# Performance work log

Measured on AMD Instinct MI355X. Metric: run time of the kernel, lower is better.

## Reference

```python
import jax, jax.numpy as jnp
from jax import lax
import numpy as np

B, T, E, D, EMB, O, L, A = 32, 500, 1024, 1024, 256, 5000, 99, 512
IGNORE = -1


def setup_inputs() -> dict:
    key = jax.random.key(0)
    ks = jax.random.split(key, 32)
    hs_pad = jax.random.normal(ks[0], (B, T, E), jnp.float32)
    hlens = jax.random.randint(ks[1], (B,), 250, T + 1).astype(jnp.int32)
    hlens = hlens.at[0].set(T)
    ylens = jax.random.randint(ks[2], (B,), 50, L + 1)
    labels = jax.random.randint(ks[3], (B, L), 0, O - 1)
    ys_pad = jnp.where(jnp.arange(L)[None, :] < ylens[:, None], labels, IGNORE)

    def w(k, shape, fan):
        return jax.random.normal(k, shape, jnp.float32) / np.float32(np.sqrt(fan))

    params = dict(
        embed=w(ks[4], (O, EMB), EMB),
        W1_W=w(ks[5], (EMB, 2 * D), EMB), b1_W=jnp.zeros(2 * D, jnp.float32),
        W1_Wx=w(ks[6], (EMB, D), EMB), b1_Wx=jnp.zeros(D, jnp.float32),
        U1=w(ks[7], (D, 2 * D), D), Ux1=w(ks[8], (D, D), D),
        U2=w(ks[9], (D, 2 * D), D), b2=jnp.zeros(2 * D, jnp.float32),
        Wc=w(ks[10], (E, 2 * D), E),
        Ux2=w(ks[11], (D, D), D), bUx2=jnp.zeros(D, jnp.float32),
        Wcx=w(ks[12], (E, D), E),
        Winit=w(ks[13], (E, D), E), binit=jnp.zeros(D, jnp.float32),
        Ws=w(ks[14], (D, D), D), bs=jnp.zeros(D, jnp.float32),
        Wy=w(ks[15], (EMB, D), EMB),
        We=w(ks[16], (E, D), E),
        Wlogit=w(ks[17], (D // 2, O), D // 2), blogit=jnp.zeros(O, jnp.float32),
        Wenc=w(ks[18], (E, A), E), Wdec=w(ks[19], (D, A), D),
    )
    return {"hs_pad": hs_pad, "hlens": hlens, "ys_pad": ys_pad, **params}


def reference(hs_pad, hlens, ys_pad, embed, W1_W, b1_W, W1_Wx, b1_Wx, U1, Ux1,
              U2, b2, Wc, Ux2, bUx2, Wcx, Winit, binit, Ws, bs, Wy, We,
              Wlogit, blogit, Wenc, Wdec):
    b, t, e = hs_pad.shape
    d = U1.shape[0]
    o = Wlogit.shape[1]
    sos = eos = o - 1
    l = ys_pad.shape[1]
    olen = l + 1

    ylens = jnp.sum(ys_pad != IGNORE, axis=1)                       # [B]
    ys_in = jnp.concatenate(
        [jnp.full((b, 1), sos, ys_pad.dtype),
         jnp.where(ys_pad == IGNORE, eos, ys_pad)], axis=1)          # [B, olen]
    ymask = (jnp.arange(olen)[None, :] < (ylens + 1)[:, None]).astype(hs_pad.dtype)
    cmask = (jnp.arange(t)[None, :] < hlens[:, None]).astype(hs_pad.dtype)

    # mean_init_state: sums all frames (incl. padding, as in original), / hlens
    h0 = (hs_pad.sum(1) / hlens[:, None].astype(hs_pad.dtype)) @ Winit + binit
    alpha0 = cmask / (cmask.sum(1, keepdims=True) + 1e-8)

    eys = embed[ys_in]                                               # [B, olen, EMB]
    sb_ = eys @ W1_W + b1_W                                          # rnn1_W(eys)
    sbx = eys @ W1_Wx + b1_Wx                                        # rnn1_Wx(eys)

    enc_att = jnp.tanh(hs_pad @ Wenc)                                # [B,T,A] precomputed

    def step(carry, xs):
        h_, alpha = carry
        x_, xx_, m_, sb = xs
        # first GRU cell
        pre1 = jax.nn.sigmoid(h_ @ U1 + x_)
        r1, u1 = pre1[:, :d], pre1[:, d:]
        h1 = jnp.tanh((h_ @ Ux1) * r1 + xx_)
        h1 = u1 * h_ + (1.0 - u1) * h1
        h1 = m_[:, None] * h1 + (1.0 - m_)[:, None] * h_
        # masked dot attention
        dq = jnp.tanh(h1 @ Wdec)                                     # [B,A]
        en = jnp.einsum('bta,ba->bt', enc_att, dq)
        en = jnp.where(cmask > 0, en, -1e9)
        w_att = jax.nn.softmax(en, axis=1)
        c = jnp.einsum('bt,bte->be', w_att, hs_pad)                  # [B,E]
        # second (conditioned) GRU cell
        pre2 = jax.nn.sigmoid(h1 @ U2 + b2 + c @ Wc)
        r2, u2 = pre2[:, :d], pre2[:, d:]
        h2 = jnp.tanh((h1 @ Ux2 + bUx2) * r2 + c @ Wcx)
        h2 = u2 * h1 + (1.0 - u2) * h2
        h2 = m_[:, None] * h2 + (1.0 - m_)[:, None] * h1
        # maxout classifier
        logit = h2 @ Ws + bs + sb @ Wy + c @ We                      # [B,D]
        logit = logit.reshape(b, d // 2, 2).max(-1)
        probs = jax.nn.softmax(logit @ Wlogit + blogit, axis=-1)
        return (h2, w_att), probs

    xs = (jnp.swapaxes(sb_, 0, 1), jnp.swapaxes(sbx, 0, 1),
          ymask.T, jnp.swapaxes(eys, 0, 1))
    _, out = lax.scan(step, (h0, alpha0), xs)                        # [olen,B,O]
    return jnp.swapaxes(out, 0, 1)                                   # [B,olen,O]
```

## Files before the change

kernel.cpp:

```cpp
#include <hip/hip_runtime.h>
#include <math.h>

static constexpr int Bb   = 32;
static constexpr int Tt   = 500;
static constexpr int Ee   = 1024;
static constexpr int EMBc = 256;
static constexpr int Oo   = 5000;
static constexpr int Llen = 99;
static constexpr int OLEN = 100;
static constexpr int Aa   = 512;


__global__ void k_ylens(const int* __restrict__ ys, int* __restrict__ ylens) {
    int b = threadIdx.x;
    if (b < Bb) {
        int c = 0;
        for (int i = 0; i < Llen; i++) c += (ys[b * Llen + i] != -1) ? 1 : 0;
        ylens[b] = c;
    }
}

__global__ void k_embed(const int* __restrict__ ys, const float* __restrict__ embed,
                        float* __restrict__ eys) {
    int blk = blockIdx.x;
    int b = blk / OLEN, i = blk % OLEN;
    int id = Oo - 1;
    if (i > 0) {
        int v = ys[b * Llen + i - 1];
        id = (v == -1) ? (Oo - 1) : v;
    }
    eys[(size_t)(b * OLEN + i) * EMBc + threadIdx.x] = embed[(size_t)id * EMBc + threadIdx.x];
}

__global__ void k_hmean(const float* __restrict__ hs, const int* __restrict__ hlens,
                        float* __restrict__ hm) {
    int b = blockIdx.y;
    int e = blockIdx.x * 256 + threadIdx.x;
    float sum = 0.f;
    for (int t = 0; t < Tt; t++) sum += hs[((size_t)b * Tt + t) * Ee + e];
    hm[(size_t)b * Ee + e] = sum / (float)hlens[b];
}

template <int ACT>
__global__ void k_gemm_tiled(const float* __restrict__ Amat, const float* __restrict__ W,
                             const float* __restrict__ bias, float* __restrict__ C,
                             int M, int K, int N) {
    __shared__ float As[16][132];
    __shared__ float Wt[16][68];
    const int tid = threadIdx.x;
    const int row0 = blockIdx.y * 128;
    const int col0 = blockIdx.x * 64;
    const int ty = tid >> 4, tx = tid & 15;
    float acc[8][4] = {};
    for (int kk = 0; kk < K; kk += 16) {
#pragma unroll
        for (int rr = 0; rr < 128; rr += 64) {
            int r = rr + (tid >> 2);
            int c4 = (tid & 3) * 4;
            float4 v = make_float4(0.f, 0.f, 0.f, 0.f);
            if (row0 + r < M) v = *(const float4*)(&Amat[(size_t)(row0 + r) * K + kk + c4]);
            As[c4 + 0][r] = v.x; As[c4 + 1][r] = v.y; As[c4 + 2][r] = v.z; As[c4 + 3][r] = v.w;
        }
        for (int i = tid; i < 16 * 64; i += 256)
            Wt[i >> 6][i & 63] = W[(size_t)(kk + (i >> 6)) * N + col0 + (i & 63)];
        __syncthreads();
#pragma unroll
        for (int k = 0; k < 16; k++) {
            float a[8], bbv[4];
#pragma unroll
            for (int i = 0; i < 8; i++) a[i] = As[k][ty * 8 + i];
#pragma unroll
            for (int j = 0; j < 4; j++) bbv[j] = Wt[k][tx * 4 + j];
#pragma unroll
            for (int i = 0; i < 8; i++)
#pragma unroll
                for (int j = 0; j < 4; j++) acc[i][j] += a[i] * bbv[j];
        }
        __syncthreads();
    }
#pragma unroll
    for (int i = 0; i < 8; i++) {
        int r = row0 + ty * 8 + i;
        if (r < M) {
#pragma unroll
            for (int j = 0; j < 4; j++) {
                int cc = col0 + tx * 4 + j;
                float v = acc[i][j];
                if (bias) v += bias[cc];
                if (ACT == 1) v = tanhf(v);
                C[(size_t)r * N + cc] = v;
            }
        }
    }
}


template <int KC>
__global__ void k_gemm3(const float* __restrict__ x, int ldx,
                        const float* __restrict__ Wga, const float* __restrict__ Wgb,
                        const float* __restrict__ Wxa, const float* __restrict__ Wxb,
                        int kSeg, float* __restrict__ P) {
    __shared__ float xs[Bb][KC];
    const int tid = threadIdx.x;
    const int kc = blockIdx.y;
    const int k0 = kc * KC;
    for (int i = tid; i < Bb * KC; i += 256) {
        int bb = i / KC, k = i - bb * KC;
        xs[bb][k] = x[(size_t)bb * ldx + k0 + k];
    }
    __syncthreads();
    const int tx = tid & 63, ty = tid >> 6;
    const int j = blockIdx.x * 64 + tx;
    const int b0 = ty * 8;
    const bool seg0 = (k0 < kSeg);
    const float* Wg = seg0 ? Wga : Wgb;
    const float* Wx = seg0 ? Wxa : Wxb;
    const int kbase = seg0 ? k0 : (k0 - kSeg);
    float ag[8] = {}, au[8] = {}, ax[8] = {};
    for (int kk = 0; kk < KC; kk++) {
        const float* wgr = Wg + (size_t)(kbase + kk) * 2048;
        const float* wxr = Wx + (size_t)(kbase + kk) * 1024;
        float wg0 = wgr[j], wg1 = wgr[j + 1024], wx0 = wxr[j];
#pragma unroll
        for (int i = 0; i < 8; i++) {
            float xv = xs[b0 + i][kk];
            ag[i] += xv * wg0;
            au[i] += xv * wg1;
            ax[i] += xv * wx0;
        }
    }
#pragma unroll
    for (int i = 0; i < 8; i++) {
        P[(((size_t)kc * 3 + 0) * Bb + b0 + i) * 1024 + j] = ag[i];
        P[(((size_t)kc * 3 + 1) * Bb + b0 + i) * 1024 + j] = au[i];
        P[(((size_t)kc * 3 + 2) * Bb + b0 + i) * 1024 + j] = ax[i];
    }
}

template <int KC>
__global__ void k_gemm1(const float* __restrict__ x, int ldx,
                        const float* __restrict__ Wa, const float* __restrict__ Wb,
                        int kSeg, int N, float* __restrict__ P) {
    __shared__ float xs[Bb][KC];
    const int tid = threadIdx.x;
    const int kc = blockIdx.y;
    const int k0 = kc * KC;
    for (int i = tid; i < Bb * KC; i += 256) {
        int bb = i / KC, k = i - bb * KC;
        xs[bb][k] = x[(size_t)bb * ldx + k0 + k];
    }
    __syncthreads();
    const int tx = tid & 63, ty = tid >> 6;
    const int j = blockIdx.x * 64 + tx;
    const int b0 = ty * 8;
    const bool seg0 = (k0 < kSeg);
    const float* W = seg0 ? Wa : Wb;
    const int kbase = seg0 ? k0 : (k0 - kSeg);
    float acc[8] = {};
    for (int kk = 0; kk < KC; kk++) {
        float w = W[(size_t)(kbase + kk) * N + j];
#pragma unroll
        for (int i = 0; i < 8; i++) acc[i] += xs[b0 + i][kk] * w;
    }
#pragma unroll
    for (int i = 0; i < 8; i++) P[((size_t)kc * Bb + b0 + i) * N + j] = acc[i];
}

__global__ void k_comb1(const float* __restrict__ P, const float* __restrict__ sb,
                        const float* __restrict__ sbx, const float* __restrict__ h,
                        const int* __restrict__ ylens, float* __restrict__ x23, int s) {
    int gid = blockIdx.x * 256 + threadIdx.x;
    int b = gid >> 10, j = gid & 1023;
    float s0 = 0, s1 = 0, sx = 0;
#pragma unroll
    for (int kc = 0; kc < 16; kc++) {
        s0 += P[(((size_t)kc * 3 + 0) * Bb + b) * 1024 + j];
        s1 += P[(((size_t)kc * 3 + 1) * Bb + b) * 1024 + j];
        sx += P[(((size_t)kc * 3 + 2) * Bb + b) * 1024 + j];
    }
    float r = 1.f / (1.f + expf(-(s0 + sb[((size_t)b * OLEN + s) * 2048 + j])));
    float u = 1.f / (1.f + expf(-(s1 + sb[((size_t)b * OLEN + s) * 2048 + 1024 + j])));
    float ht = tanhf(sx * r + sbx[((size_t)b * OLEN + s) * 1024 + j]);
    float hp = h[(size_t)b * 1024 + j];
    float h1 = u * hp + (1.f - u) * ht;
    float m = (s < ylens[b] + 1) ? 1.f : 0.f;
    h1 = m * h1 + (1.f - m) * hp;
    x23[(size_t)b * 2048 + j] = h1;
}

__global__ void k_en(const float* __restrict__ pd, const float* __restrict__ enc,
                     float* __restrict__ en, float* __restrict__ x23) {
    __shared__ float dqs[Aa];
    const int tid = threadIdx.x;
    const int b = blockIdx.y, tt = blockIdx.x;
    if (tid < 128) x23[(size_t)b * 2048 + 1024 + tt * 128 + tid] = 0.f;
    for (int jj = tid; jj < Aa; jj += 256) {
        float sum = 0;
#pragma unroll
        for (int kc = 0; kc < 16; kc++) sum += pd[((size_t)kc * Bb + b) * Aa + jj];
        dqs[jj] = tanhf(sum);
    }
    __syncthreads();
    const int tx = tid & 63, ty = tid >> 6;
    for (int t2 = 0; t2 < 64; t2 += 4) {
        int t = tt * 64 + t2 + ty;
        if (t < Tt) {
            float acc = 0;
            const float* er = enc + ((size_t)b * Tt + t) * Aa;
#pragma unroll
            for (int i = 0; i < 8; i++) acc += er[tx + 64 * i] * dqs[tx + 64 * i];
#pragma unroll
            for (int off = 32; off > 0; off >>= 1) acc += __shfl_down(acc, off, 64);
            if (tx == 0) en[(size_t)b * 512 + t] = acc;
        }
    }
}

__global__ void k_softc(const float* __restrict__ en, const float* __restrict__ hs,
                        const int* __restrict__ hlens, float* __restrict__ x23) {
    __shared__ float wts[Tt];
    __shared__ float red[128];
    const int tid = threadIdx.x;
    const int b = blockIdx.z;
    const int hlen = hlens[b];
    float mx = -1e30f;
    for (int t = tid; t < hlen; t += 128) mx = fmaxf(mx, en[(size_t)b * 512 + t]);
    red[tid] = mx;
    __syncthreads();
    for (int w = 64; w > 0; w >>= 1) {
        if (tid < w) red[tid] = fmaxf(red[tid], red[tid + w]);
        __syncthreads();
    }
    mx = red[0];
    __syncthreads();
    float ps = 0;
    for (int t = tid; t < Tt; t += 128) {
        float w = 0.f;
        if (t < hlen) w = expf(en[(size_t)b * 512 + t] - mx);
        wts[t] = w;
        ps += w;
    }
    red[tid] = ps;
    __syncthreads();
    for (int w = 64; w > 0; w >>= 1) {
        if (tid < w) red[tid] += red[tid + w];
        __syncthreads();
    }
    float inv = 1.f / red[0];
    __syncthreads();
    for (int t = tid; t < Tt; t += 128) wts[t] *= inv;
    __syncthreads();

    const int e0 = blockIdx.x * 512 + tid * 4;
    const int tc = blockIdx.y;
    int tstart = tc * 125;
    int tend = tstart + 125;
    if (tend > hlen) tend = hlen;
    float4 a0 = make_float4(0, 0, 0, 0), a1 = make_float4(0, 0, 0, 0);
    float4 a2 = make_float4(0, 0, 0, 0), a3 = make_float4(0, 0, 0, 0);
    int t = tstart;
    for (; t + 3 < tend; t += 4) {
        float w0 = wts[t], w1 = wts[t + 1], w2 = wts[t + 2], w3 = wts[t + 3];
        float4 h0 = *(const float4*)(&hs[((size_t)b * Tt + t) * Ee + e0]);
        float4 h1 = *(const float4*)(&hs[((size_t)b * Tt + t + 1) * Ee + e0]);
        float4 h2 = *(const float4*)(&hs[((size_t)b * Tt + t + 2) * Ee + e0]);
        float4 h3 = *(const float4*)(&hs[((size_t)b * Tt + t + 3) * Ee + e0]);
        a0.x += w0 * h0.x; a0.y += w0 * h0.y; a0.z += w0 * h0.z; a0.w += w0 * h0.w;
        a1.x += w1 * h1.x; a1.y += w1 * h1.y; a1.z += w1 * h1.z; a1.w += w1 * h1.w;
        a2.x += w2 * h2.x; a2.y += w2 * h2.y; a2.z += w2 * h2.z; a2.w += w2 * h2.w;
        a3.x += w3 * h3.x; a3.y += w3 * h3.y; a3.z += w3 * h3.z; a3.w += w3 * h3.w;
    }
    for (; t < tend; t++) {
        float w = wts[t];
        float4 hv = *(const float4*)(&hs[((size_t)b * Tt + t) * Ee + e0]);
        a0.x += w * hv.x; a0.y += w * hv.y; a0.z += w * hv.z; a0.w += w * hv.w;
    }
    a0.x += a1.x + a2.x + a3.x;
    a0.y += a1.y + a2.y + a3.y;
    a0.z += a1.z + a2.z + a3.z;
    a0.w += a1.w + a2.w + a3.w;
    float* cdst = &x23[(size_t)b * 2048 + 1024 + e0];
    atomicAdd(cdst + 0, a0.x);
    atomicAdd(cdst + 1, a0.y);
    atomicAdd(cdst + 2, a0.z);
    atomicAdd(cdst + 3, a0.w);
}

__global__ void k_comb2(const float* __restrict__ P, const float* __restrict__ b2,
                        const float* __restrict__ bUx2, const int* __restrict__ ylens,
                        float* __restrict__ x23, float* __restrict__ h, int s) {
    int gid = blockIdx.x * 256 + threadIdx.x;
    int b = gid >> 10, j = gid & 1023;
    float s0 = 0, s1 = 0, xa = 0, xb = 0;
#pragma unroll
    for (int kc = 0; kc < 16; kc++) {
        s0 += P[(((size_t)kc * 3 + 0) * Bb + b) * 1024 + j];
        s1 += P[(((size_t)kc * 3 + 1) * Bb + b) * 1024 + j];
        float px = P[(((size_t)kc * 3 + 2) * Bb + b) * 1024 + j];
        if (kc < 8) xa += px; else xb += px;
    }
    float r = 1.f / (1.f + expf(-(s0 + b2[j])));
    float u = 1.f / (1.f + expf(-(s1 + b2[1024 + j])));
    float h2t = tanhf((xa + bUx2[j]) * r + xb);
    float h1v = x23[(size_t)b * 2048 + j];
    float h2 = u * h1v + (1.f - u) * h2t;
    float m = (s < ylens[b] + 1) ? 1.f : 0.f;
    h2 = m * h2 + (1.f - m) * h1v;
    x23[(size_t)b * 2048 + j] = h2;
    h[(size_t)b * 1024 + j] = h2;
}


__global__ void k_gemmL(const float* __restrict__ x23a, const float* __restrict__ eys,
                        const float* __restrict__ Ws, const float* __restrict__ We,
                        const float* __restrict__ Wy, const float* __restrict__ bs,
                        float* __restrict__ mo) {
    __shared__ float As[16][132];
    __shared__ float Wt[16][68];
    const int tid = threadIdx.x;
    const int row0 = blockIdx.y * 128;
    const int col0 = blockIdx.x * 64;
    const int ty = tid >> 4, tx = tid & 15;
    float acc[8][4] = {};
    for (int kk = 0; kk < 2304; kk += 16) {
#pragma unroll
        for (int rr = 0; rr < 128; rr += 64) {
            int rl = rr + (tid >> 2);
            int r = row0 + rl;
            int c4 = (tid & 3) * 4;
            float4 v;
            if (kk < 2048) {
                v = *(const float4*)(&x23a[(size_t)r * 2048 + kk + c4]);
            } else {
                int bI = r & 31, sI = r >> 5;
                v = *(const float4*)(&eys[((size_t)bI * OLEN + sI) * EMBc + (kk - 2048) + c4]);
            }
            As[c4 + 0][rl] = v.x; As[c4 + 1][rl] = v.y; As[c4 + 2][rl] = v.z; As[c4 + 3][rl] = v.w;
        }
        for (int i = tid; i < 16 * 64; i += 256) {
            int rowk = kk + (i >> 6);
            const float* wr = (rowk < 1024) ? &Ws[(size_t)rowk * 1024]
                             : (rowk < 2048) ? &We[(size_t)(rowk - 1024) * 1024]
                                             : &Wy[(size_t)(rowk - 2048) * 1024];
            Wt[i >> 6][i & 63] = wr[col0 + (i & 63)];
        }
        __syncthreads();
#pragma unroll
        for (int k = 0; k < 16; k++) {
            float a[8], bbv[4];
#pragma unroll
            for (int i = 0; i < 8; i++) a[i] = As[k][ty * 8 + i];
#pragma unroll
            for (int j = 0; j < 4; j++) bbv[j] = Wt[k][tx * 4 + j];
#pragma unroll
            for (int i = 0; i < 8; i++)
#pragma unroll
                for (int j = 0; j < 4; j++) acc[i][j] += a[i] * bbv[j];
        }
        __syncthreads();
    }
#pragma unroll
    for (int i = 0; i < 8; i++) {
        int r = row0 + ty * 8 + i;
#pragma unroll
        for (int p = 0; p < 2; p++) {
            int c = col0 + tx * 4 + p * 2;
            float v0 = acc[i][p * 2 + 0] + bs[c + 0];
            float v1 = acc[i][p * 2 + 1] + bs[c + 1];
            mo[(size_t)r * 512 + (c >> 1)] = fmaxf(v0, v1);
        }
    }
}

__global__ void k_gemmZ(const float* __restrict__ mo, const float* __restrict__ Wl,
                        const float* __restrict__ bl, float* __restrict__ out) {
    __shared__ float As[16][132];
    __shared__ float Wt[16][68];
    const int tid = threadIdx.x;
    const int row0 = blockIdx.y * 128;
    const int col0 = blockIdx.x * 64;
    const int ty = tid >> 4, tx = tid & 15;
    float acc[8][4] = {};
    for (int kk = 0; kk < 512; kk += 16) {
#pragma unroll
        for (int rr = 0; rr < 128; rr += 64) {
            int rl = rr + (tid >> 2);
            int r = row0 + rl;
            int c4 = (tid & 3) * 4;
            float4 v = *(const float4*)(&mo[(size_t)r * 512 + kk + c4]);
            As[c4 + 0][rl] = v.x; As[c4 + 1][rl] = v.y; As[c4 + 2][rl] = v.z; As[c4 + 3][rl] = v.w;
        }
        for (int i = tid; i < 16 * 64; i += 256) {
            int c = col0 + (i & 63);
            if (c > Oo - 1) c = Oo - 1;
            Wt[i >> 6][i & 63] = Wl[(size_t)(kk + (i >> 6)) * Oo + c];
        }
        __syncthreads();
#pragma unroll
        for (int k = 0; k < 16; k++) {
            float a[8], bbv[4];
#pragma unroll
            for (int i = 0; i < 8; i++) a[i] = As[k][ty * 8 + i];
#pragma unroll
            for (int j = 0; j < 4; j++) bbv[j] = Wt[k][tx * 4 + j];
#pragma unroll
            for (int i = 0; i < 8; i++)
#pragma unroll
                for (int j = 0; j < 4; j++) acc[i][j] += a[i] * bbv[j];
        }
        __syncthreads();
    }
#pragma unroll
    for (int i = 0; i < 8; i++) {
        int r = row0 + ty * 8 + i;
        int bI = r & 31, sI = r >> 5;
        float* zr = out + ((size_t)bI * OLEN + sI) * Oo;
#pragma unroll
        for (int j = 0; j < 4; j++) {
            int c = col0 + tx * 4 + j;
            if (c < Oo) zr[c] = acc[i][j] + bl[c];
        }
    }
}

__global__ void k_osm(float* __restrict__ out) {
    __shared__ float red[256];
    __shared__ float ev[Oo];
    const int tid = threadIdx.x;
    const int r = blockIdx.x;
    const int bI = r & 31, sI = r >> 5;
    float* zr = out + ((size_t)bI * OLEN + sI) * Oo;
    float mx = -1e30f;
    for (int i = tid; i < Oo; i += 256) mx = fmaxf(mx, zr[i]);
    red[tid] = mx;
    __syncthreads();
    for (int w = 128; w > 0; w >>= 1) {
        if (tid < w) red[tid] = fmaxf(red[tid], red[tid + w]);
        __syncthreads();
    }
    mx = red[0];
    __syncthreads();
    float ps = 0;
    for (int i = tid; i < Oo; i += 256) {
        float e = expf(zr[i] - mx);
        ev[i] = e;
        ps += e;
    }
    red[tid] = ps;
    __syncthreads();
    for (int w = 128; w > 0; w >>= 1) {
        if (tid < w) red[tid] += red[tid + w];
        __syncthreads();
    }
    float inv = 1.f / red[0];
    for (int i = tid; i < Oo; i += 256) zr[i] = ev[i] * inv;
}


extern "C" void kernel_launch(void* const* d_in, const int* in_sizes, int n_in,
                              void* d_out, int out_size, void* d_ws, size_t ws_size,
                              hipStream_t stream) {
    const float* hs    = (const float*)d_in[0];
    const int*   hlens = (const int*)d_in[1];
    const int*   ys    = (const int*)d_in[2];
    const float* embed = (const float*)d_in[3];
    const float* W1_W  = (const float*)d_in[4];
    const float* b1_W  = (const float*)d_in[5];
    const float* W1_Wx = (const float*)d_in[6];
    const float* b1_Wx = (const float*)d_in[7];
    const float* U1    = (const float*)d_in[8];
    const float* Ux1   = (const float*)d_in[9];
    const float* U2    = (const float*)d_in[10];
    const float* b2    = (const float*)d_in[11];
    const float* Wc    = (const float*)d_in[12];
    const float* Ux2   = (const float*)d_in[13];
    const float* bUx2  = (const float*)d_in[14];
    const float* Wcx   = (const float*)d_in[15];
    const float* Winit = (const float*)d_in[16];
    const float* binit = (const float*)d_in[17];
    const float* Ws    = (const float*)d_in[18];
    const float* bs    = (const float*)d_in[19];
    const float* Wy    = (const float*)d_in[20];
    const float* We    = (const float*)d_in[21];
    const float* Wlog  = (const float*)d_in[22];
    const float* blog  = (const float*)d_in[23];
    const float* Wenc  = (const float*)d_in[24];
    const float* Wdec  = (const float*)d_in[25];
    float* out = (float*)d_out;
    float* wsp = (float*)d_ws;

    float* enc_att = wsp;
    float* sb      = enc_att + (size_t)Bb * Tt * Aa;
    float* sbx     = sb      + (size_t)Bb * OLEN * 2048;
    float* eys     = sbx     + (size_t)Bb * OLEN * 1024;
    float* h       = eys     + (size_t)Bb * OLEN * EMBc;
    float* en      = h       + (size_t)Bb * 1024;
    float* pd      = en      + (size_t)Bb * 512;
    float* p3      = pd      + (size_t)16 * Bb * 512;
    int*   ylens   = (int*)(p3 + (size_t)16 * 3 * Bb * 1024);
    float* hm      = pd;
    float* mo      = pd;
    float* xall    = out;

    k_ylens<<<1, 64, 0, stream>>>(ys, ylens);
    k_embed<<<Bb * OLEN, EMBc, 0, stream>>>(ys, embed, eys);
    k_hmean<<<dim3(4, Bb), 256, 0, stream>>>(hs, hlens, hm);
    k_gemm_tiled<0><<<dim3(16, 1), 256, 0, stream>>>(hm, Winit, binit, h, Bb, 1024, 1024);
    k_gemm_tiled<0><<<dim3(32, 25), 256, 0, stream>>>(eys, W1_W, b1_W, sb, Bb * OLEN, EMBc, 2048);
    k_gemm_tiled<0><<<dim3(16, 25), 256, 0, stream>>>(eys, W1_Wx, b1_Wx, sbx, Bb * OLEN, EMBc, 1024);
    k_gemm_tiled<1><<<dim3(8, 125), 256, 0, stream>>>(hs, Wenc, nullptr, enc_att, Bb * Tt, Ee, Aa);

    for (int s = 0; s < OLEN; s++) {
        float* x23s = xall + (size_t)s * Bb * 2048;
        k_gemm3<64><<<dim3(16, 16), 256, 0, stream>>>(h, 1024, U1, U1, Ux1, Ux1, 1024, p3);
        k_comb1<<<128, 256, 0, stream>>>(p3, sb, sbx, h, ylens, x23s, s);
        k_gemm1<64><<<dim3(8, 16), 256, 0, stream>>>(x23s, 2048, Wdec, Wdec, 1024, 512, pd);
        k_en<<<dim3(8, Bb), 256, 0, stream>>>(pd, enc_att, en, x23s);
        k_softc<<<dim3(2, 4, Bb), 128, 0, stream>>>(en, hs, hlens, x23s);
        k_gemm3<128><<<dim3(16, 16), 256, 0, stream>>>(x23s, 2048, U2, Wc, Ux2, Wcx, 1024, p3);
        k_comb2<<<128, 256, 0, stream>>>(p3, b2, bUx2, ylens, x23s, h, s);
    }

    k_gemmL<<<dim3(16, 25), 256, 0, stream>>>(xall, eys, Ws, We, Wy, bs, mo);
    k_gemmZ<<<dim3(79, 25), 256, 0, stream>>>(mo, Wlog, blog, out);
    k_osm<<<Bb * OLEN, 256, 0, stream>>>(out);
}
```

Before: 12.54 ms.

## Fuse per-step recurrence kernels into one persistent cooperative kernel with grid syncs

Replaces the 700 small per-step kernel launches of the decoder recurrence with a single cooperative persistent kernel of 256 blocks. Each stage becomes a block-strided task loop, and stages are separated by grid-wide barriers. The context-buffer zeroing moves into the first stage, and the softmax/context kernel is reworked for 256 threads per block covering the full E width. The aim is to remove launch overhead and inter-kernel gaps, at the cost of seven grid.sync barriers per step and occupancy limited to one block per CU.

```diff
diff --git a/kernel.cpp b/kernel.cpp
--- a/kernel.cpp
+++ b/kernel.cpp
@@ -1,5 +1,8 @@
 #include <hip/hip_runtime.h>
+#include <hip/hip_cooperative_groups.h>
 #include <math.h>
+
+namespace cg = cooperative_groups;
 
 static constexpr int Bb   = 32;
 static constexpr int Tt   = 500;
@@ -96,21 +99,20 @@
 
 
 template <int KC>
-__global__ void k_gemm3(const float* __restrict__ x, int ldx,
-                        const float* __restrict__ Wga, const float* __restrict__ Wgb,
-                        const float* __restrict__ Wxa, const float* __restrict__ Wxb,
-                        int kSeg, float* __restrict__ P) {
-    __shared__ float xs[Bb][KC];
-    const int tid = threadIdx.x;
-    const int kc = blockIdx.y;
+__device__ __forceinline__ void gemm3_body(const float* __restrict__ x, int ldx,
+                                           const float* __restrict__ Wga, const float* __restrict__ Wgb,
+                                           const float* __restrict__ Wxa, const float* __restrict__ Wxb,
+                                           int kSeg, float* __restrict__ P, int jb, int kc,
+                                           float* __restrict__ xs) {
+    const int tid = threadIdx.x;
     const int k0 = kc * KC;
     for (int i = tid; i < Bb * KC; i += 256) {
         int bb = i / KC, k = i - bb * KC;
-        xs[bb][k] = x[(size_t)bb * ldx + k0 + k];
+        xs[bb * KC + k] = x[(size_t)bb * ldx + k0 + k];
     }
     __syncthreads();
     const int tx = tid & 63, ty = tid >> 6;
-    const int j = blockIdx.x * 64 + tx;
+    const int j = jb * 64 + tx;
     const int b0 = ty * 8;
     const bool seg0 = (k0 < kSeg);
     const float* Wg = seg0 ? Wga : Wgb;
@@ -123,7 +125,7 @@
         float wg0 = wgr[j], wg1 = wgr[j + 1024], wx0 = wxr[j];
 #pragma unroll
         for (int i = 0; i < 8; i++) {
-            float xv = xs[b0 + i][kk];
+            float xv = xs[(b0 + i) * KC + kk];
             ag[i] += xv * wg0;
             au[i] += xv * wg1;
             ax[i] += xv * wx0;
@@ -135,179 +137,210 @@
         P[(((size_t)kc * 3 + 1) * Bb + b0 + i) * 1024 + j] = au[i];
         P[(((size_t)kc * 3 + 2) * Bb + b0 + i) * 1024 + j] = ax[i];
     }
+    __syncthreads();
 }
 
 template <int KC>
-__global__ void k_gemm1(const float* __restrict__ x, int ldx,
-                        const float* __restrict__ Wa, const float* __restrict__ Wb,
-                        int kSeg, int N, float* __restrict__ P) {
-    __shared__ float xs[Bb][KC];
-    const int tid = threadIdx.x;
-    const int kc = blockIdx.y;
+__device__ __forceinline__ void gemm1_body(const float* __restrict__ x, int ldx,
+                                           const float* __restrict__ W, int N,
+                                           float* __restrict__ P, int jb, int kc,
+                                           float* __restrict__ xs) {
+    const int tid = threadIdx.x;
     const int k0 = kc * KC;
     for (int i = tid; i < Bb * KC; i += 256) {
         int bb = i / KC, k = i - bb * KC;
-        xs[bb][k] = x[(size_t)bb * ldx + k0 + k];
+        xs[bb * KC + k] = x[(size_t)bb * ldx + k0 + k];
     }
     __syncthreads();
     const int tx = tid & 63, ty = tid >> 6;
-    const int j = blockIdx.x * 64 + tx;
+    const int j = jb * 64 + tx;
     const int b0 = ty * 8;
-    const bool seg0 = (k0 < kSeg);
-    const float* W = seg0 ? Wa : Wb;
-    const int kbase = seg0 ? k0 : (k0 - kSeg);
     float acc[8] = {};
     for (int kk = 0; kk < KC; kk++) {
-        float w = W[(size_t)(kbase + kk) * N + j];
-#pragma unroll
-        for (int i = 0; i < 8; i++) acc[i] += xs[b0 + i][kk] * w;
+        float w = W[(size_t)(k0 + kk) * N + j];
+#pragma unroll
+        for (int i = 0; i < 8; i++) acc[i] += xs[(b0 + i) * KC + kk] * w;
     }
 #pragma unroll
     for (int i = 0; i < 8; i++) P[((size_t)kc * Bb + b0 + i) * N + j] = acc[i];
-}
-
-__global__ void k_comb1(const float* __restrict__ P, const float* __restrict__ sb,
-                        const float* __restrict__ sbx, const float* __restrict__ h,
-                        const int* __restrict__ ylens, float* __restrict__ x23, int s) {
-    int gid = blockIdx.x * 256 + threadIdx.x;
-    int b = gid >> 10, j = gid & 1023;
-    float s0 = 0, s1 = 0, sx = 0;
-#pragma unroll
-    for (int kc = 0; kc < 16; kc++) {
-        s0 += P[(((size_t)kc * 3 + 0) * Bb + b) * 1024 + j];
-        s1 += P[(((size_t)kc * 3 + 1) * Bb + b) * 1024 + j];
-        sx += P[(((size_t)kc * 3 + 2) * Bb + b) * 1024 + j];
-    }
-    float r = 1.f / (1.f + expf(-(s0 + sb[((size_t)b * OLEN + s) * 2048 + j])));
-    float u = 1.f / (1.f + expf(-(s1 + sb[((size_t)b * OLEN + s) * 2048 + 1024 + j])));
-    float ht = tanhf(sx * r + sbx[((size_t)b * OLEN + s) * 1024 + j]);
-    float hp = h[(size_t)b * 1024 + j];
-    float h1 = u * hp + (1.f - u) * ht;
-    float m = (s < ylens[b] + 1) ? 1.f : 0.f;
-    h1 = m * h1 + (1.f - m) * hp;
-    x23[(size_t)b * 2048 + j] = h1;
-}
-
-__global__ void k_en(const float* __restrict__ pd, const float* __restrict__ enc,
-                     float* __restrict__ en, float* __restrict__ x23) {
-    __shared__ float dqs[Aa];
-    const int tid = threadIdx.x;
-    const int b = blockIdx.y, tt = blockIdx.x;
-    if (tid < 128) x23[(size_t)b * 2048 + 1024 + tt * 128 + tid] = 0.f;
-    for (int jj = tid; jj < Aa; jj += 256) {
-        float sum = 0;
-#pragma unroll
-        for (int kc = 0; kc < 16; kc++) sum += pd[((size_t)kc * Bb + b) * Aa + jj];
-        dqs[jj] = tanhf(sum);
-    }
-    __syncthreads();
-    const int tx = tid & 63, ty = tid >> 6;
-    for (int t2 = 0; t2 < 64; t2 += 4) {
-        int t = tt * 64 + t2 + ty;
-        if (t < Tt) {
-            float acc = 0;
-            const float* er = enc + ((size_t)b * Tt + t) * Aa;
-#pragma unroll
-            for (int i = 0; i < 8; i++) acc += er[tx + 64 * i] * dqs[tx + 64 * i];
-#pragma unroll
-            for (int off = 32; off > 0; off >>= 1) acc += __shfl_down(acc, off, 64);
-            if (tx == 0) en[(size_t)b * 512 + t] = acc;
-        }
-    }
-}
-
-__global__ void k_softc(const float* __restrict__ en, const float* __restrict__ hs,
-                        const int* __restrict__ hlens, float* __restrict__ x23) {
-    __shared__ float wts[Tt];
-    __shared__ float red[128];
-    const int tid = threadIdx.x;
-    const int b = blockIdx.z;
-    const int hlen = hlens[b];
-    float mx = -1e30f;
-    for (int t = tid; t < hlen; t += 128) mx = fmaxf(mx, en[(size_t)b * 512 + t]);
-    red[tid] = mx;
-    __syncthreads();
-    for (int w = 64; w > 0; w >>= 1) {
-        if (tid < w) red[tid] = fmaxf(red[tid], red[tid + w]);
-        __syncthreads();
-    }
-    mx = red[0];
-    __syncthreads();
-    float ps = 0;
-    for (int t = tid; t < Tt; t += 128) {
-        float w = 0.f;
-        if (t < hlen) w = expf(en[(size_t)b * 512 + t] - mx);
-        wts[t] = w;
-        ps += w;
-    }
-    red[tid] = ps;
-    __syncthreads();
-    for (int w = 64; w > 0; w >>= 1) {
-        if (tid < w) red[tid] += red[tid + w];
-        __syncthreads();
-    }
-    float inv = 1.f / red[0];
-    __syncthreads();
-    for (int t = tid; t < Tt; t += 128) wts[t] *= inv;
-    __syncthreads();
-
-    const int e0 = blockIdx.x * 512 + tid * 4;
-    const int tc = blockIdx.y;
-    int tstart = tc * 125;
-    int tend = tstart + 125;
-    if (tend > hlen) tend = hlen;
-    float4 a0 = make_float4(0, 0, 0, 0), a1 = make_float4(0, 0, 0, 0);
-    float4 a2 = make_float4(0, 0, 0, 0), a3 = make_float4(0, 0, 0, 0);
-    int t = tstart;
-    for (; t + 3 < tend; t += 4) {
-        float w0 = wts[t], w1 = wts[t + 1], w2 = wts[t + 2], w3 = wts[t + 3];
-        float4 h0 = *(const float4*)(&hs[((size_t)b * Tt + t) * Ee + e0]);
-        float4 h1 = *(const float4*)(&hs[((size_t)b * Tt + t + 1) * Ee + e0]);
-        float4 h2 = *(const float4*)(&hs[((size_t)b * Tt + t + 2) * Ee + e0]);
-        float4 h3 = *(const float4*)(&hs[((size_t)b * Tt + t + 3) * Ee + e0]);
-        a0.x += w0 * h0.x; a0.y += w0 * h0.y; a0.z += w0 * h0.z; a0.w += w0 * h0.w;
-        a1.x += w1 * h1.x; a1.y += w1 * h1.y; a1.z += w1 * h1.z; a1.w += w1 * h1.w;
-        a2.x += w2 * h2.x; a2.y += w2 * h2.y; a2.z += w2 * h2.z; a2.w += w2 * h2.w;
-        a3.x += w3 * h3.x; a3.y += w3 * h3.y; a3.z += w3 * h3.z; a3.w += w3 * h3.w;
-    }
-    for (; t < tend; t++) {
-        float w = wts[t];
-        float4 hv = *(const float4*)(&hs[((size_t)b * Tt + t) * Ee + e0]);
-        a0.x += w * hv.x; a0.y += w * hv.y; a0.z += w * hv.z; a0.w += w * hv.w;
-    }
-    a0.x += a1.x + a2.x + a3.x;
-    a0.y += a1.y + a2.y + a3.y;
-    a0.z += a1.z + a2.z + a3.z;
-    a0.w += a1.w + a2.w + a3.w;
-    float* cdst = &x23[(size_t)b * 2048 + 1024 + e0];
-    atomicAdd(cdst + 0, a0.x);
-    atomicAdd(cdst + 1, a0.y);
-    atomicAdd(cdst + 2, a0.z);
-    atomicAdd(cdst + 3, a0.w);
-}
-
-__global__ void k_comb2(const float* __restrict__ P, const float* __restrict__ b2,
-                        const float* __restrict__ bUx2, const int* __restrict__ ylens,
-                        float* __restrict__ x23, float* __restrict__ h, int s) {
-    int gid = blockIdx.x * 256 + threadIdx.x;
-    int b = gid >> 10, j = gid & 1023;
-    float s0 = 0, s1 = 0, xa = 0, xb = 0;
-#pragma unroll
-    for (int kc = 0; kc < 16; kc++) {
-        s0 += P[(((size_t)kc * 3 + 0) * Bb + b) * 1024 + j];
-        s1 += P[(((size_t)kc * 3 + 1) * Bb + b) * 1024 + j];
-        float px = P[(((size_t)kc * 3 + 2) * Bb + b) * 1024 + j];
-        if (kc < 8) xa += px; else xb += px;
-    }
-    float r = 1.f / (1.f + expf(-(s0 + b2[j])));
-    float u = 1.f / (1.f + expf(-(s1 + b2[1024 + j])));
-    float h2t = tanhf((xa + bUx2[j]) * r + xb);
-    float h1v = x23[(size_t)b * 2048 + j];
-    float h2 = u * h1v + (1.f - u) * h2t;
-    float m = (s < ylens[b] + 1) ? 1.f : 0.f;
-    h2 = m * h2 + (1.f - m) * h1v;
-    x23[(size_t)b * 2048 + j] = h2;
-    h[(size_t)b * 1024 + j] = h2;
+    __syncthreads();
+}
+
+__global__ __launch_bounds__(256, 1) void k_recur(
+    const float* __restrict__ hs, const int* __restrict__ hlens, const int* __restrict__ ylens,
+    const float* __restrict__ U1, const float* __restrict__ Ux1,
+    const float* __restrict__ U2, const float* __restrict__ b2, const float* __restrict__ Wc,
+    const float* __restrict__ Ux2, const float* __restrict__ bUx2, const float* __restrict__ Wcx,
+    const float* __restrict__ Wdec, const float* __restrict__ sb, const float* __restrict__ sbx,
+    const float* __restrict__ enc_att,
+    float* __restrict__ h, float* __restrict__ xall, float* __restrict__ en,
+    float* __restrict__ pd, float* __restrict__ p3) {
+    cg::grid_group grid = cg::this_grid();
+    __shared__ float smem[4608];
+    const int tid = threadIdx.x;
+    const int nb = gridDim.x;
+
+    for (int s = 0; s < OLEN; s++) {
+        float* x23s = xall + (size_t)s * Bb * 2048;
+
+        for (int task = blockIdx.x; task < 384; task += nb) {
+            if (task < 256) {
+                gemm3_body<64>(h, 1024, U1, U1, Ux1, Ux1, 1024, p3, task & 15, task >> 4, smem);
+            } else {
+                int idx = (task - 256) * 256 + tid;
+                x23s[((idx >> 10) * 2048) + 1024 + (idx & 1023)] = 0.f;
+            }
+        }
+        grid.sync();
+
+        for (int task = blockIdx.x; task < 128; task += nb) {
+            int gid = task * 256 + tid;
+            int b = gid >> 10, j = gid & 1023;
+            float s0 = 0, s1 = 0, sx = 0;
+#pragma unroll
+            for (int kc = 0; kc < 16; kc++) {
+                s0 += p3[(((size_t)kc * 3 + 0) * Bb + b) * 1024 + j];
+                s1 += p3[(((size_t)kc * 3 + 1) * Bb + b) * 1024 + j];
+                sx += p3[(((size_t)kc * 3 + 2) * Bb + b) * 1024 + j];
+            }
+            float r = 1.f / (1.f + expf(-(s0 + sb[((size_t)b * OLEN + s) * 2048 + j])));
+            float u = 1.f / (1.f + expf(-(s1 + sb[((size_t)b * OLEN + s) * 2048 + 1024 + j])));
+            float ht = tanhf(sx * r + sbx[((size_t)b * OLEN + s) * 1024 + j]);
+            float hp = h[(size_t)b * 1024 + j];
+            float h1 = u * hp + (1.f - u) * ht;
+            float m = (s < ylens[b] + 1) ? 1.f : 0.f;
+            h1 = m * h1 + (1.f - m) * hp;
+            x23s[(size_t)b * 2048 + j] = h1;
+        }
+        grid.sync();
+
+        for (int task = blockIdx.x; task < 128; task += nb)
+            gemm1_body<64>(x23s, 2048, Wdec, 512, pd, task & 7, task >> 3, smem);
+        grid.sync();
+
+        for (int task = blockIdx.x; task < 256; task += nb) {
+            int b = task >> 3, tt = task & 7;
+            float* dqs = smem;
+            for (int jj = tid; jj < Aa; jj += 256) {
+                float sum = 0;
+#pragma unroll
+                for (int kc = 0; kc < 16; kc++) sum += pd[((size_t)kc * Bb + b) * Aa + jj];
+                dqs[jj] = tanhf(sum);
+            }
+            __syncthreads();
+            const int tx = tid & 63, ty = tid >> 6;
+            for (int t2 = 0; t2 < 64; t2 += 4) {
+                int t = tt * 64 + t2 + ty;
+                if (t < Tt) {
+                    float acc = 0;
+                    const float* er = enc_att + ((size_t)b * Tt + t) * Aa;
+#pragma unroll
+                    for (int i = 0; i < 8; i++) acc += er[tx + 64 * i] * dqs[tx + 64 * i];
+#pragma unroll
+                    for (int off = 32; off > 0; off >>= 1) acc += __shfl_down(acc, off, 64);
+                    if (tx == 0) en[(size_t)b * 512 + t] = acc;
+                }
+            }
+            __syncthreads();
+        }
+        grid.sync();
+
+        for (int task = blockIdx.x; task < 128; task += nb) {
+            int b = task >> 2, tc = task & 3;
+            float* wts = smem;
+            float* red = smem + 512;
+            const int hlen = hlens[b];
+            float mx = -1e30f;
+            for (int t = tid; t < hlen; t += 256) mx = fmaxf(mx, en[(size_t)b * 512 + t]);
+            red[tid] = mx;
+            __syncthreads();
+            for (int w = 128; w > 0; w >>= 1) {
+                if (tid < w) red[tid] = fmaxf(red[tid], red[tid + w]);
+                __syncthreads();
+            }
+            mx = red[0];
+            __syncthreads();
+            float ps = 0;
+            for (int t = tid; t < Tt; t += 256) {
+                float w = 0.f;
+                if (t < hlen) w = expf(en[(size_t)b * 512 + t] - mx);
+                wts[t] = w;
+                ps += w;
+            }
+            red[tid] = ps;
+            __syncthreads();
+            for (int w = 128; w > 0; w >>= 1) {
+                if (tid < w) red[tid] += red[tid + w];
+                __syncthreads();
+            }
+            float inv = 1.f / red[0];
+            __syncthreads();
+            for (int t = tid; t < Tt; t += 256) wts[t] *= inv;
+            __syncthreads();
+
+            const int e0 = tid * 4;
+            int tstart = tc * 125;
+            int tend = tstart + 125;
+            if (tend > hlen) tend = hlen;
+            float4 a0 = make_float4(0, 0, 0, 0), a1 = make_float4(0, 0, 0, 0);
+            float4 a2 = make_float4(0, 0, 0, 0), a3 = make_float4(0, 0, 0, 0);
+            int t = tstart;
+            for (; t + 3 < tend; t += 4) {
+                float w0 = wts[t], w1 = wts[t + 1], w2 = wts[t + 2], w3 = wts[t + 3];
+                float4 h0 = *(const float4*)(&hs[((size_t)b * Tt + t) * Ee + e0]);
+                float4 h1 = *(const float4*)(&hs[((size_t)b * Tt + t + 1) * Ee + e0]);
+                float4 h2 = *(const float4*)(&hs[((size_t)b * Tt + t + 2) * Ee + e0]);
+                float4 h3 = *(const float4*)(&hs[((size_t)b * Tt + t + 3) * Ee + e0]);
+                a0.x += w0 * h0.x; a0.y += w0 * h0.y; a0.z += w0 * h0.z; a0.w += w0 * h0.w;
+                a1.x += w1 * h1.x; a1.y += w1 * h1.y; a1.z += w1 * h1.z; a1.w += w1 * h1.w;
+                a2.x += w2 * h2.x; a2.y += w2 * h2.y; a2.z += w2 * h2.z; a2.w += w2 * h2.w;
+                a3.x += w3 * h3.x; a3.y += w3 * h3.y; a3.z += w3 * h3.z; a3.w += w3 * h3.w;
+            }
+            for (; t < tend; t++) {
+                float w = wts[t];
+                float4 hv = *(const float4*)(&hs[((size_t)b * Tt + t) * Ee + e0]);
+                a0.x += w * hv.x; a0.y += w * hv.y; a0.z += w * hv.z; a0.w += w * hv.w;
+            }
+            a0.x += a1.x + a2.x + a3.x;
+            a0.y += a1.y + a2.y + a3.y;
+            a0.z += a1.z + a2.z + a3.z;
+            a0.w += a1.w + a2.w + a3.w;
+            float* cdst = &x23s[(size_t)b * 2048 + 1024 + e0];
+            atomicAdd(cdst + 0, a0.x);
+            atomicAdd(cdst + 1, a0.y);
+            atomicAdd(cdst + 2, a0.z);
+            atomicAdd(cdst + 3, a0.w);
+            __syncthreads();
+        }
+        grid.sync();
+
+        for (int task = blockIdx.x; task < 256; task += nb)
+            gemm3_body<128>(x23s, 2048, U2, Wc, Ux2, Wcx, 1024, p3, task & 15, task >> 4, smem);
+        grid.sync();
+
+        for (int task = blockIdx.x; task < 128; task += nb) {
+            int gid = task * 256 + tid;
+            int b = gid >> 10, j = gid & 1023;
+            float s0 = 0, s1 = 0, xa = 0, xb = 0;
+#pragma unroll
+            for (int kc = 0; kc < 16; kc++) {
+                s0 += p3[(((size_t)kc * 3 + 0) * Bb + b) * 1024 + j];
+                s1 += p3[(((size_t)kc * 3 + 1) * Bb + b) * 1024 + j];
+                float px = p3[(((size_t)kc * 3 + 2) * Bb + b) * 1024 + j];
+                if (kc < 8) xa += px; else xb += px;
+            }
+            float r = 1.f / (1.f + expf(-(s0 + b2[j])));
+            float u = 1.f / (1.f + expf(-(s1 + b2[1024 + j])));
+            float h2t = tanhf((xa + bUx2[j]) * r + xb);
+            float h1v = x23s[(size_t)b * 2048 + j];
+            float h2 = u * h1v + (1.f - u) * h2t;
+            float m = (s < ylens[b] + 1) ? 1.f : 0.f;
+            h2 = m * h2 + (1.f - m) * h1v;
+            x23s[(size_t)b * 2048 + j] = h2;
+            h[(size_t)b * 1024 + j] = h2;
+        }
+        grid.sync();
+    }
 }
 
 
@@ -510,15 +543,16 @@
     k_gemm_tiled<0><<<dim3(16, 25), 256, 0, stream>>>(eys, W1_Wx, b1_Wx, sbx, Bb * OLEN, EMBc, 1024);
     k_gemm_tiled<1><<<dim3(8, 125), 256, 0, stream>>>(hs, Wenc, nullptr, enc_att, Bb * Tt, Ee, Aa);
 
-    for (int s = 0; s < OLEN; s++) {
-        float* x23s = xall + (size_t)s * Bb * 2048;
-        k_gemm3<64><<<dim3(16, 16), 256, 0, stream>>>(h, 1024, U1, U1, Ux1, Ux1, 1024, p3);
-        k_comb1<<<128, 256, 0, stream>>>(p3, sb, sbx, h, ylens, x23s, s);
-        k_gemm1<64><<<dim3(8, 16), 256, 0, stream>>>(x23s, 2048, Wdec, Wdec, 1024, 512, pd);
-        k_en<<<dim3(8, Bb), 256, 0, stream>>>(pd, enc_att, en, x23s);
-        k_softc<<<dim3(2, 4, Bb), 128, 0, stream>>>(en, hs, hlens, x23s);
-        k_gemm3<128><<<dim3(16, 16), 256, 0, stream>>>(x23s, 2048, U2, Wc, Ux2, Wcx, 1024, p3);
-        k_comb2<<<128, 256, 0, stream>>>(p3, b2, bUx2, ylens, x23s, h, s);
+    {
+        void* cargs[] = {
+            (void*)&hs, (void*)&hlens, (void*)&ylens,
+            (void*)&U1, (void*)&Ux1,
+            (void*)&U2, (void*)&b2, (void*)&Wc,
+            (void*)&Ux2, (void*)&bUx2, (void*)&Wcx,
+            (void*)&Wdec, (void*)&sb, (void*)&sbx, (void*)&enc_att,
+            (void*)&h, (void*)&xall, (void*)&en, (void*)&pd, (void*)&p3
+        };
+        hipLaunchCooperativeKernel((const void*)k_recur, dim3(256), dim3(256), cargs, 0, stream);
     }
 
     k_gemmL<<<dim3(16, 25), 256, 0, stream>>>(xall, eys, Ws, We, Wy, bs, mo);
```

Result: slower. 31.87 ms (+154.1%).
